# Kernel tuning notes

Measured on AMD Instinct MI355X. Metric: run time of the kernel, lower is better.

## Reference

```python
import jax, jax.numpy as jnp
import numpy as np

N_EMBED = 1024
N_HEADS = 16
HEAD_SIZE = N_EMBED // N_HEADS


def setup_inputs() -> dict:
    key = jax.random.key(0)
    ks = jax.random.split(key, 9)
    d = N_EMBED
    s = 1.0 / np.sqrt(d)
    return {
        "x": jax.random.normal(ks[0], (2, 2048, d), dtype=jnp.float32),
        "Wq": jax.random.uniform(ks[1], (d, d), jnp.float32, -s, s),
        "bq": jax.random.uniform(ks[2], (d,), jnp.float32, -s, s),
        "Wk": jax.random.uniform(ks[3], (d, d), jnp.float32, -s, s),
        "bk": jax.random.uniform(ks[4], (d,), jnp.float32, -s, s),
        "Wv": jax.random.uniform(ks[5], (d, d), jnp.float32, -s, s),
        "bv": jax.random.uniform(ks[6], (d,), jnp.float32, -s, s),
        "Wo": jax.random.uniform(ks[7], (d, d), jnp.float32, -s, s),
        "bo": jax.random.uniform(ks[8], (d,), jnp.float32, -s, s),
    }


def reference(x, Wq, bq, Wk, bk, Wv, bv, Wo, bo):
    B, T, D = x.shape
    H, Hd = N_HEADS, HEAD_SIZE
    # projections (torch Linear: x @ W^T + b; here W stored already transposed)
    q = (x @ Wq + bq).reshape(B, T, H, Hd).transpose(0, 2, 1, 3)  # [B,H,T,Hd]
    k = (x @ Wk + bk).reshape(B, T, H, Hd).transpose(0, 2, 1, 3)
    v = (x @ Wv + bv).reshape(B, T, H, Hd).transpose(0, 2, 1, 3)
    scores = jnp.einsum("bhqd,bhkd->bhqk", q, k) * (Hd ** -0.5)  # [B,H,T,T]
    causal = jnp.tril(jnp.ones((T, T), dtype=bool))
    scores = jnp.where(causal[None, None], scores, -jnp.inf)
    probs = jax.nn.softmax(scores, axis=-1)
    out = jnp.einsum("bhqk,bhkd->bhqd", probs, v)  # [B,H,T,Hd]
    out = out.transpose(0, 2, 1, 3).reshape(B, T, D)
    return out @ Wo + bo
```

## Files before the change

### kernel.cpp

```cpp
#include <hip/hip_runtime.h>
#include <cstdint>
#include <cstddef>

typedef __bf16 bf16;
typedef __bf16 bf16x4 __attribute__((ext_vector_type(4)));
typedef __bf16 bf16x8 __attribute__((ext_vector_type(8)));
typedef float  f32x4  __attribute__((ext_vector_type(4)));
typedef float  f32x16 __attribute__((ext_vector_type(16)));

#define B_  2
#define T_  2048
#define D_  1024
#define H_  16
#define HD_ 64
#define M_  (B_ * T_)
#define NQB 32

#define GLOAD_LDS(gsrc, ldst) \
    __builtin_amdgcn_global_load_lds( \
        (const __attribute__((address_space(1))) void*)(gsrc), \
        (__attribute__((address_space(3))) void*)(ldst), 16, 0, 0)

__global__ void prep_kernel(
    const float* __restrict__ x,  bf16* __restrict__ xb,
    const float* __restrict__ W0, bf16* __restrict__ T0,
    const float* __restrict__ W1, bf16* __restrict__ T1,
    const float* __restrict__ W2, bf16* __restrict__ T2,
    const float* __restrict__ W3, bf16* __restrict__ T3)
{
    if (blockIdx.z == 4) {
        const int linear = blockIdx.y * 32 + blockIdx.x;
        const int base = linear * 4096 + threadIdx.x * 4;
        #pragma unroll
        for (int u = 0; u < 4; ++u) {
            const int i = base + u * 1024;
            const float4 v = *reinterpret_cast<const float4*>(x + i);
            bf16x4 o = { (bf16)v.x, (bf16)v.y, (bf16)v.z, (bf16)v.w };
            *reinterpret_cast<bf16x4*>(xb + i) = o;
        }
        return;
    }
    __shared__ float tile[32][33];
    const float* W = blockIdx.z == 0 ? W0 : blockIdx.z == 1 ? W1 : blockIdx.z == 2 ? W2 : W3;
    bf16*       Wt = blockIdx.z == 0 ? T0 : blockIdx.z == 1 ? T1 : blockIdx.z == 2 ? T2 : T3;
    const int tx = threadIdx.x & 31, ty = threadIdx.x >> 5;
    const int bx = blockIdx.x * 32, by = blockIdx.y * 32;
    #pragma unroll
    for (int r = 0; r < 32; r += 8)
        tile[ty + r][tx] = W[(size_t)(by + ty + r) * D_ + bx + tx];
    __syncthreads();
    #pragma unroll
    for (int r = 0; r < 32; r += 8)
        Wt[(size_t)(bx + ty + r) * D_ + by + tx] = (bf16)tile[tx][ty + r];
}

__device__ __forceinline__ void gemm_128_2ph(
    const bf16* __restrict__ A, const bf16* __restrict__ Bt,
    int m0, int n0, bf16 (*As)[128][64], bf16 (*Bs)[128][64], f32x16 acc[2][2])
{
    constexpr int K = D_;
    constexpr int NK = K / 64;
    const int tid  = threadIdx.x;
    const int wave = tid >> 6, lane = tid & 63;
    const int l5 = lane & 31, hi = lane >> 5;
    const int wr = wave >> 1, wc = wave & 1;

    const int rseg = lane >> 3;
    const int srcc = (lane & 7) ^ rseg;

    auto stage = [&](int b, int k0) {
        #pragma unroll
        for (int cc = 0; cc < 4; ++cc) {
            const int c   = wave * 4 + cc;
            const int row = c * 8 + rseg;
            GLOAD_LDS(A  + (size_t)(m0 + row) * K + k0 + srcc * 8, &As[b][c * 8][0]);
            GLOAD_LDS(Bt + (size_t)(n0 + row) * K + k0 + srcc * 8, &Bs[b][c * 8][0]);
        }
    };

    stage(0, 0);
    __syncthreads();

    #pragma unroll 1
    for (int t = 0; t < NK; ++t) {
        const int cur = t & 1;
        if (t + 1 < NK) stage(cur ^ 1, (t + 1) * 64);

        bf16x8 af[2][4], bfr[2][4];
        #pragma unroll
        for (int mi = 0; mi < 2; ++mi)
            #pragma unroll
            for (int ks = 0; ks < 4; ++ks) {
                const int row = wr * 64 + mi * 32 + l5;
                af[mi][ks] = *reinterpret_cast<const bf16x8*>(
                    &As[cur][row][((ks * 2 + hi) ^ (row & 7)) * 8]);
            }
        #pragma unroll
        for (int nj = 0; nj < 2; ++nj)
            #pragma unroll
            for (int ks = 0; ks < 4; ++ks) {
                const int row = wc * 64 + nj * 32 + l5;
                bfr[nj][ks] = *reinterpret_cast<const bf16x8*>(
                    &Bs[cur][row][((ks * 2 + hi) ^ (row & 7)) * 8]);
            }
        __builtin_amdgcn_s_setprio(1);
        #pragma unroll
        for (int mi = 0; mi < 2; ++mi)
            #pragma unroll
            for (int nj = 0; nj < 2; ++nj)
                #pragma unroll
                for (int ks = 0; ks < 4; ++ks)
                    acc[mi][nj] = __builtin_amdgcn_mfma_f32_32x32x16_bf16(
                        af[mi][ks], bfr[nj][ks], acc[mi][nj], 0, 0, 0);
        __builtin_amdgcn_s_setprio(0);
        __syncthreads();
    }
}

__global__ __launch_bounds__(256, 2) void qkv128_kernel(
    const bf16* __restrict__ xb,
    const bf16* __restrict__ WqT, const float* __restrict__ bq, bf16* __restrict__ Qo,
    const bf16* __restrict__ WkT, const float* __restrict__ bk, bf16* __restrict__ Ko,
    const bf16* __restrict__ WvT, const float* __restrict__ bv, bf16* __restrict__ Vt)
{
    __shared__ bf16 As[2][128][64];
    __shared__ bf16 Bs[2][128][64];

    const int bid = blockIdx.x;
    const int swz = (bid & 7) * 96 + (bid >> 3);

    const bf16 *Aop, *Bop;
    const float *bias;
    bf16 *outp;
    float scale = 1.0f;
    int m0, n0, mode;
    if (swz < 512) {
        const int bm = swz & 31, bn = swz >> 5;
        m0 = bm * 128;
        Aop = xb;
        if (bn < 8) { Bop = WqT; n0 = bn * 128;       bias = bq; outp = Qo; scale = 0.125f; }
        else        { Bop = WkT; n0 = (bn - 8) * 128; bias = bk; outp = Ko; }
        mode = 0;
    } else {
        const int v = swz - 512, bm = v & 7, bn = v >> 3;
        m0 = bm * 128; n0 = bn * 128;
        Aop = WvT; Bop = xb; bias = bv; outp = Vt; mode = 1;
    }

    f32x16 acc[2][2] = {};
    gemm_128_2ph(Aop, Bop, m0, n0, As, Bs, acc);

    const int lane = threadIdx.x & 63, wave = threadIdx.x >> 6;
    const int l5 = lane & 31, hi = lane >> 5;
    const int wr = wave >> 1, wc = wave & 1;
    if (mode == 0) {
        #pragma unroll
        for (int mi = 0; mi < 2; ++mi)
            #pragma unroll
            for (int nj = 0; nj < 2; ++nj)
                #pragma unroll
                for (int q = 0; q < 16; ++q) {
                    const int m = m0 + wr * 64 + mi * 32 + (q & 3) + 8 * (q >> 2) + 4 * hi;
                    const int n = n0 + wc * 64 + nj * 32 + l5;
                    const float val = (acc[mi][nj][q] + bias[n]) * scale;
                    const int b = m >> 11, t = m & (T_ - 1);
                    const int h = n >> 6, hd = n & 63;
                    outp[((size_t)((b * H_ + h) * T_ + t)) * HD_ + hd] = (bf16)val;
                }
    } else {
        #pragma unroll
        for (int mi = 0; mi < 2; ++mi)
            #pragma unroll
            for (int nj = 0; nj < 2; ++nj)
                #pragma unroll
                for (int q = 0; q < 16; ++q) {
                    const int d = m0 + wr * 64 + mi * 32 + (q & 3) + 8 * (q >> 2) + 4 * hi;
                    const int n = n0 + wc * 64 + nj * 32 + l5;
                    const float val = acc[mi][nj][q] + bias[d];
                    const int b = n >> 11, t = n & (T_ - 1);
                    outp[((size_t)(b * D_ + d)) * T_ + t] = (bf16)val;
                }
    }
}

__global__ __launch_bounds__(256, 2) void gemm_out_kernel(
    const bf16* __restrict__ A, const bf16* __restrict__ WoT,
    const float* __restrict__ bo, float* __restrict__ Out)
{
    __shared__ bf16 As[2][128][64];
    __shared__ bf16 Bs[2][128][64];
    const int m0 = blockIdx.x * 128, n0 = blockIdx.y * 128;

    f32x16 acc[2][2] = {};
    gemm_128_2ph(A, WoT, m0, n0, As, Bs, acc);

    const int lane = threadIdx.x & 63, wave = threadIdx.x >> 6;
    const int l5 = lane & 31, hi = lane >> 5;
    const int wr = wave >> 1, wc = wave & 1;
    #pragma unroll
    for (int mi = 0; mi < 2; ++mi)
        #pragma unroll
        for (int nj = 0; nj < 2; ++nj)
            #pragma unroll
            for (int q = 0; q < 16; ++q) {
                const int m = m0 + wr * 64 + mi * 32 + (q & 3) + 8 * (q >> 2) + 4 * hi;
                const int n = n0 + wc * 64 + nj * 32 + l5;
                Out[(size_t)m * D_ + n] = acc[mi][nj][q] + bo[n];
            }
}

__global__ __launch_bounds__(256) void attn_kernel(
    const bf16* __restrict__ Q, const bf16* __restrict__ K,
    const bf16* __restrict__ Vt, bf16* __restrict__ Out)
{
    const int bid = blockIdx.x;
    const int xcd = bid & 7, j = bid >> 3;
    const int bh  = xcd * 4 + (j >> 4);
    const int pr  = j & 15;

    const int tid = threadIdx.x, wave = tid >> 6, lane = tid & 63;
    const int lr = lane & 15, lg = lane >> 4;
    const size_t kbase = (size_t)bh * T_ * HD_;
    const size_t vbase = (size_t)bh * HD_ * T_;

    __shared__ bf16 Ks[2][64][64];
    __shared__ bf16 Vs[2][64][64];
    __shared__ bf16 Ps[4][16][72];

    auto stage = [&](int sb, int kt) {
        const int kv0 = kt * 64;
        const int rseg = lane >> 3;
        const int srcw = (lane & 7) ^ rseg;
        #pragma unroll
        for (int cc = 0; cc < 2; ++cc) {
            const int seg = wave * 2 + cc;
            const int row = seg * 8 + rseg;
            GLOAD_LDS(K  + kbase + (size_t)(kv0 + row) * HD_ + srcw * 8, &Ks[sb][seg * 8][0]);
            GLOAD_LDS(Vt + vbase + (size_t)row * T_ + kv0 + srcw * 8,    &Vs[sb][seg * 8][0]);
        }
    };
    auto kfrag = [&](int sb, int row, int chunk) {
        return *reinterpret_cast<const bf16x8*>(&Ks[sb][row][(chunk ^ (row & 7)) * 8]);
    };
    auto vfrag = [&](int sb, int row, int chunk) {
        return *reinterpret_cast<const bf16x8*>(&Vs[sb][row][(chunk ^ (row & 7)) * 8]);
    };

    #pragma unroll 1
    for (int half = 0; half < 2; ++half) {
        const int qb = half == 0 ? pr : (NQB - 1 - pr);
        const int q0 = qb * 64;
        const int nt = qb + 1;
        const int qw = wave * 16;

        bf16x8 qf[2];
        {
            const bf16* qrow = Q + kbase + (size_t)(q0 + qw + lr) * HD_;
            qf[0] = *reinterpret_cast<const bf16x8*>(qrow + lg * 8);
            qf[1] = *reinterpret_cast<const bf16x8*>(qrow + 32 + lg * 8);
        }

        float m_s = -1e30f, l_s = 0.f;
        f32x4 o_acc[4] = {};

        stage(0, 0);
        __syncthreads();

        #pragma unroll 1
        for (int t = 0; t < nt; ++t) {
            const int cur = t & 1;
            if (t + 1 < nt) stage(cur ^ 1, t + 1);

            const int kv0 = t * 64;
            f32x4 s[4] = {};
            __builtin_amdgcn_s_setprio(1);
            #pragma unroll
            for (int n16 = 0; n16 < 4; ++n16)
                #pragma unroll
                for (int kk = 0; kk < 2; ++kk)
                    s[n16] = __builtin_amdgcn_mfma_f32_16x16x32_bf16(
                        kfrag(cur, n16 * 16 + lr, kk * 4 + lg), qf[kk], s[n16], 0, 0, 0);
            __builtin_amdgcn_s_setprio(0);
            if (t == qb) {
                #pragma unroll
                for (int n16 = 0; n16 < 4; ++n16)
                    #pragma unroll
                    for (int r = 0; r < 4; ++r)
                        if (kv0 + n16 * 16 + lg * 4 + r > q0 + qw + lr)
                            s[n16][r] = -1e30f;
            }
            float mx = s[0][0];
            #pragma unroll
            for (int n16 = 0; n16 < 4; ++n16)
                #pragma unroll
                for (int r = 0; r < 4; ++r)
                    mx = fmaxf(mx, s[n16][r]);
            mx = fmaxf(mx, __shfl_xor(mx, 16));
            mx = fmaxf(mx, __shfl_xor(mx, 32));
            if (__any(mx > m_s + 8.0f)) {
                const float mnew  = fmaxf(m_s, mx);
                const float alpha = __expf(m_s - mnew);
                #pragma unroll
                for (int r = 0; r < 4; ++r) {
                    const float a = __shfl(alpha, lg * 4 + r);
                    #pragma unroll
                    for (int nd = 0; nd < 4; ++nd) o_acc[nd][r] *= a;
                }
                l_s *= alpha;
                m_s = mnew;
            }
            float rs = 0.f;
            #pragma unroll
            for (int n16 = 0; n16 < 4; ++n16) {
                bf16x4 pw;
                #pragma unroll
                for (int r = 0; r < 4; ++r) {
                    const float p = __expf(s[n16][r] - m_s);
                    rs += p;
                    pw[r] = (bf16)p;
                }
                *reinterpret_cast<bf16x4*>(&Ps[wave][lr][n16 * 16 + lg * 4]) = pw;
            }
            rs += __shfl_xor(rs, 16);
            rs += __shfl_xor(rs, 32);
            l_s += rs;
            __builtin_amdgcn_s_setprio(1);
            #pragma unroll
            for (int ks = 0; ks < 2; ++ks) {
                const bf16x8 pa = *reinterpret_cast<const bf16x8*>(&Ps[wave][lr][ks * 32 + lg * 8]);
                #pragma unroll
                for (int nd = 0; nd < 4; ++nd)
                    o_acc[nd] = __builtin_amdgcn_mfma_f32_16x16x32_bf16(
                        pa, vfrag(cur, nd * 16 + lr, ks * 4 + lg), o_acc[nd], 0, 0, 0);
            }
            __builtin_amdgcn_s_setprio(0);
            __syncthreads();
        }

        const int b = bh >> 4, h = bh & 15;
        const float linv = 1.0f / l_s;
        #pragma unroll
        for (int r = 0; r < 4; ++r) {
            const float li = __shfl(linv, lg * 4 + r);
            const int q = q0 + qw + lg * 4 + r;
            #pragma unroll
            for (int nd = 0; nd < 4; ++nd) {
                const int d = nd * 16 + lr;
                Out[((size_t)(b * T_ + q)) * D_ + h * HD_ + d] = (bf16)(o_acc[nd][r] * li);
            }
        }
    }
}

extern "C" void kernel_launch(void* const* d_in, const int* in_sizes, int n_in,
                              void* d_out, int out_size, void* d_ws, size_t ws_size,
                              hipStream_t stream) {
    const float* x  = (const float*)d_in[0];
    const float* Wq = (const float*)d_in[1];
    const float* bq = (const float*)d_in[2];
    const float* Wk = (const float*)d_in[3];
    const float* bk = (const float*)d_in[4];
    const float* Wv = (const float*)d_in[5];
    const float* bv = (const float*)d_in[6];
    const float* Wo = (const float*)d_in[7];
    const float* bo = (const float*)d_in[8];
    float* out = (float*)d_out;

    char* ws = (char*)d_ws;
    bf16* xb   = (bf16*)(ws);
    bf16* WqT  = (bf16*)(ws + ( 8u << 20));
    bf16* WkT  = (bf16*)(ws + (10u << 20));
    bf16* WvT  = (bf16*)(ws + (12u << 20));
    bf16* WoT  = (bf16*)(ws + (14u << 20));
    bf16* Qb   = (bf16*)(ws + (16u << 20));
    bf16* Kb   = (bf16*)(ws + (24u << 20));
    bf16* Vtb  = (bf16*)(ws + (32u << 20));
    bf16* attn = (bf16*)(ws + (40u << 20));

    prep_kernel<<<dim3(32, 32, 5), 256, 0, stream>>>(
        x, xb, Wq, WqT, Wk, WkT, Wv, WvT, Wo, WoT);

    qkv128_kernel<<<768, 256, 0, stream>>>(xb, WqT, bq, Qb, WkT, bk, Kb, WvT, bv, Vtb);

    attn_kernel<<<512, 256, 0, stream>>>(Qb, Kb, Vtb, attn);

    gemm_out_kernel<<<dim3(32, 8), 256, 0, stream>>>(attn, WoT, bo, out);
}
```

Measured before the change: 126.9 us.

## Fold log2e into Q scale, split attention per q-block, retile output GEMM

The Q projection scale now includes log2(e), so the attention softmax uses exp2f directly, and the lazy-rescale threshold is scaled to match. The attention kernel drops the paired-block loop: it launches one block per (head, q-block), largest blocks first, doubling the grid to 1024 and relying on the hardware scheduler to balance the causal work. The output projection GEMM becomes a custom 64x128 tile kernel using 32x32x16 MFMA with XCD-aware swizzling and 512 blocks, aiming for better CU occupancy. More blocks add launch overhead and reload Q per block, and grid-level scheduling may balance the uneven causal work less well than the explicit pairing did.

```diff
diff --git a/kernel.cpp b/kernel.cpp
--- a/kernel.cpp
+++ b/kernel.cpp
@@ -138,7 +138,8 @@
         const int bm = swz & 31, bn = swz >> 5;
         m0 = bm * 128;
         Aop = xb;
-        if (bn < 8) { Bop = WqT; n0 = bn * 128;       bias = bq; outp = Qo; scale = 0.125f; }
+        if (bn < 8) { Bop = WqT; n0 = bn * 128;       bias = bq; outp = Qo;
+                      scale = 0.125f * 1.44269504f; }
         else        { Bop = WkT; n0 = (bn - 8) * 128; bias = bk; outp = Ko; }
         mode = 0;
     } else {
@@ -187,26 +188,78 @@
     const bf16* __restrict__ A, const bf16* __restrict__ WoT,
     const float* __restrict__ bo, float* __restrict__ Out)
 {
-    __shared__ bf16 As[2][128][64];
+    constexpr int K = D_;
+    constexpr int NK = K / 64;
+    __shared__ bf16 As[2][64][64];
     __shared__ bf16 Bs[2][128][64];
-    const int m0 = blockIdx.x * 128, n0 = blockIdx.y * 128;
-
-    f32x16 acc[2][2] = {};
-    gemm_128_2ph(A, WoT, m0, n0, As, Bs, acc);
-
-    const int lane = threadIdx.x & 63, wave = threadIdx.x >> 6;
+
+    const int bid = blockIdx.x;
+    const int swz = (bid & 7) * 64 + (bid >> 3);
+    const int m0 = (swz & 63) * 64, n0 = (swz >> 6) * 128;
+
+    const int tid = threadIdx.x, wave = tid >> 6, lane = tid & 63;
     const int l5 = lane & 31, hi = lane >> 5;
-    const int wr = wave >> 1, wc = wave & 1;
+    const int rseg = lane >> 3;
+    const int srcc = (lane & 7) ^ rseg;
+
+    auto stage = [&](int b, int k0) {
+        #pragma unroll
+        for (int cc = 0; cc < 2; ++cc) {
+            const int seg = wave * 2 + cc;
+            const int row = seg * 8 + rseg;
+            GLOAD_LDS(A + (size_t)(m0 + row) * K + k0 + srcc * 8, &As[b][seg * 8][0]);
+        }
+        #pragma unroll
+        for (int cc = 0; cc < 4; ++cc) {
+            const int seg = wave * 4 + cc;
+            const int row = seg * 8 + rseg;
+            GLOAD_LDS(WoT + (size_t)(n0 + row) * K + k0 + srcc * 8, &Bs[b][seg * 8][0]);
+        }
+    };
+
+    f32x16 acc[2] = {};
+    stage(0, 0);
+    __syncthreads();
+
+    #pragma unroll 1
+    for (int t = 0; t < NK; ++t) {
+        const int cur = t & 1;
+        if (t + 1 < NK) stage(cur ^ 1, (t + 1) * 64);
+
+        bf16x8 af[2][4], bfr[4];
+        #pragma unroll
+        for (int mi = 0; mi < 2; ++mi)
+            #pragma unroll
+            for (int ks = 0; ks < 4; ++ks) {
+                const int row = mi * 32 + l5;
+                af[mi][ks] = *reinterpret_cast<const bf16x8*>(
+                    &As[cur][row][((ks * 2 + hi) ^ (row & 7)) * 8]);
+            }
+        #pragma unroll
+        for (int ks = 0; ks < 4; ++ks) {
+            const int row = wave * 32 + l5;
+            bfr[ks] = *reinterpret_cast<const bf16x8*>(
+                &Bs[cur][row][((ks * 2 + hi) ^ (row & 7)) * 8]);
+        }
+        __builtin_amdgcn_s_setprio(1);
+        #pragma unroll
+        for (int mi = 0; mi < 2; ++mi)
+            #pragma unroll
+            for (int ks = 0; ks < 4; ++ks)
+                acc[mi] = __builtin_amdgcn_mfma_f32_32x32x16_bf16(
+                    af[mi][ks], bfr[ks], acc[mi], 0, 0, 0);
+        __builtin_amdgcn_s_setprio(0);
+        __syncthreads();
+    }
+
     #pragma unroll
     for (int mi = 0; mi < 2; ++mi)
         #pragma unroll
-        for (int nj = 0; nj < 2; ++nj)
-            #pragma unroll
-            for (int q = 0; q < 16; ++q) {
-                const int m = m0 + wr * 64 + mi * 32 + (q & 3) + 8 * (q >> 2) + 4 * hi;
-                const int n = n0 + wc * 64 + nj * 32 + l5;
-                Out[(size_t)m * D_ + n] = acc[mi][nj][q] + bo[n];
-            }
+        for (int q = 0; q < 16; ++q) {
+            const int m = m0 + mi * 32 + (q & 3) + 8 * (q >> 2) + 4 * hi;
+            const int n = n0 + wave * 32 + l5;
+            Out[(size_t)m * D_ + n] = acc[mi][q] + bo[n];
+        }
 }
 
 __global__ __launch_bounds__(256) void attn_kernel(
@@ -215,8 +268,8 @@
 {
     const int bid = blockIdx.x;
     const int xcd = bid & 7, j = bid >> 3;
-    const int bh  = xcd * 4 + (j >> 4);
-    const int pr  = j & 15;
+    const int bh  = xcd * 4 + (j >> 5);
+    const int qb  = NQB - 1 - (j & 31);
 
     const int tid = threadIdx.x, wave = tid >> 6, lane = tid & 63;
     const int lr = lane & 15, lg = lane >> 4;
@@ -246,108 +299,104 @@
         return *reinterpret_cast<const bf16x8*>(&Vs[sb][row][(chunk ^ (row & 7)) * 8]);
     };
 
+    const int q0 = qb * 64;
+    const int nt = qb + 1;
+    const int qw = wave * 16;
+
+    bf16x8 qf[2];
+    {
+        const bf16* qrow = Q + kbase + (size_t)(q0 + qw + lr) * HD_;
+        qf[0] = *reinterpret_cast<const bf16x8*>(qrow + lg * 8);
+        qf[1] = *reinterpret_cast<const bf16x8*>(qrow + 32 + lg * 8);
+    }
+
+    float m_s = -1e30f, l_s = 0.f;
+    f32x4 o_acc[4] = {};
+
+    stage(0, 0);
+    __syncthreads();
+
     #pragma unroll 1
-    for (int half = 0; half < 2; ++half) {
-        const int qb = half == 0 ? pr : (NQB - 1 - pr);
-        const int q0 = qb * 64;
-        const int nt = qb + 1;
-        const int qw = wave * 16;
-
-        bf16x8 qf[2];
-        {
-            const bf16* qrow = Q + kbase + (size_t)(q0 + qw + lr) * HD_;
-            qf[0] = *reinterpret_cast<const bf16x8*>(qrow + lg * 8);
-            qf[1] = *reinterpret_cast<const bf16x8*>(qrow + 32 + lg * 8);
-        }
-
-        float m_s = -1e30f, l_s = 0.f;
-        f32x4 o_acc[4] = {};
-
-        stage(0, 0);
-        __syncthreads();
-
-        #pragma unroll 1
-        for (int t = 0; t < nt; ++t) {
-            const int cur = t & 1;
-            if (t + 1 < nt) stage(cur ^ 1, t + 1);
-
-            const int kv0 = t * 64;
-            f32x4 s[4] = {};
-            __builtin_amdgcn_s_setprio(1);
-            #pragma unroll
-            for (int n16 = 0; n16 < 4; ++n16)
-                #pragma unroll
-                for (int kk = 0; kk < 2; ++kk)
-                    s[n16] = __builtin_amdgcn_mfma_f32_16x16x32_bf16(
-                        kfrag(cur, n16 * 16 + lr, kk * 4 + lg), qf[kk], s[n16], 0, 0, 0);
-            __builtin_amdgcn_s_setprio(0);
-            if (t == qb) {
-                #pragma unroll
-                for (int n16 = 0; n16 < 4; ++n16)
-                    #pragma unroll
-                    for (int r = 0; r < 4; ++r)
-                        if (kv0 + n16 * 16 + lg * 4 + r > q0 + qw + lr)
-                            s[n16][r] = -1e30f;
-            }
-            float mx = s[0][0];
+    for (int t = 0; t < nt; ++t) {
+        const int cur = t & 1;
+        if (t + 1 < nt) stage(cur ^ 1, t + 1);
+
+        const int kv0 = t * 64;
+        f32x4 s[4] = {};
+        __builtin_amdgcn_s_setprio(1);
+        #pragma unroll
+        for (int n16 = 0; n16 < 4; ++n16)
+            #pragma unroll
+            for (int kk = 0; kk < 2; ++kk)
+                s[n16] = __builtin_amdgcn_mfma_f32_16x16x32_bf16(
+                    kfrag(cur, n16 * 16 + lr, kk * 4 + lg), qf[kk], s[n16], 0, 0, 0);
+        __builtin_amdgcn_s_setprio(0);
+        if (t == qb) {
             #pragma unroll
             for (int n16 = 0; n16 < 4; ++n16)
                 #pragma unroll
                 for (int r = 0; r < 4; ++r)
-                    mx = fmaxf(mx, s[n16][r]);
-            mx = fmaxf(mx, __shfl_xor(mx, 16));
-            mx = fmaxf(mx, __shfl_xor(mx, 32));
-            if (__any(mx > m_s + 8.0f)) {
-                const float mnew  = fmaxf(m_s, mx);
-                const float alpha = __expf(m_s - mnew);
+                    if (kv0 + n16 * 16 + lg * 4 + r > q0 + qw + lr)
+                        s[n16][r] = -1e30f;
+        }
+        float mx = s[0][0];
+        #pragma unroll
+        for (int n16 = 0; n16 < 4; ++n16)
+            #pragma unroll
+            for (int r = 0; r < 4; ++r)
+                mx = fmaxf(mx, s[n16][r]);
+        mx = fmaxf(mx, __shfl_xor(mx, 16));
+        mx = fmaxf(mx, __shfl_xor(mx, 32));
+        if (__any(mx > m_s + 11.5416f)) {
+            const float mnew  = fmaxf(m_s, mx);
+            const float alpha = exp2f(m_s - mnew);
+            #pragma unroll
+            for (int r = 0; r < 4; ++r) {
+                const float a = __shfl(alpha, lg * 4 + r);
                 #pragma unroll
-                for (int r = 0; r < 4; ++r) {
-                    const float a = __shfl(alpha, lg * 4 + r);
-                    #pragma unroll
-                    for (int nd = 0; nd < 4; ++nd) o_acc[nd][r] *= a;
-                }
-                l_s *= alpha;
-                m_s = mnew;
+                for (int nd = 0; nd < 4; ++nd) o_acc[nd][r] *= a;
             }
-            float rs = 0.f;
-            #pragma unroll
-            for (int n16 = 0; n16 < 4; ++n16) {
-                bf16x4 pw;
-                #pragma unroll
-                for (int r = 0; r < 4; ++r) {
-                    const float p = __expf(s[n16][r] - m_s);
-                    rs += p;
-                    pw[r] = (bf16)p;
-                }
-                *reinterpret_cast<bf16x4*>(&Ps[wave][lr][n16 * 16 + lg * 4]) = pw;
+            l_s *= alpha;
+            m_s = mnew;
+        }
+        float rs = 0.f;
+        #pragma unroll
+        for (int n16 = 0; n16 < 4; ++n16) {
+            bf16x4 pw;
+            #pragma unroll
+            for (int r = 0; r < 4; ++r) {
+                const float p = exp2f(s[n16][r] - m_s);
+                rs += p;
+                pw[r] = (bf16)p;
             }
-            rs += __shfl_xor(rs, 16);
-            rs += __shfl_xor(rs, 32);
-            l_s += rs;
-            __builtin_amdgcn_s_setprio(1);
-            #pragma unroll
-            for (int ks = 0; ks < 2; ++ks) {
-                const bf16x8 pa = *reinterpret_cast<const bf16x8*>(&Ps[wave][lr][ks * 32 + lg * 8]);
-                #pragma unroll
-                for (int nd = 0; nd < 4; ++nd)
-                    o_acc[nd] = __builtin_amdgcn_mfma_f32_16x16x32_bf16(
-                        pa, vfrag(cur, nd * 16 + lr, ks * 4 + lg), o_acc[nd], 0, 0, 0);
-            }
-            __builtin_amdgcn_s_setprio(0);
-            __syncthreads();
-        }
-
-        const int b = bh >> 4, h = bh & 15;
-        const float linv = 1.0f / l_s;
-        #pragma unroll
-        for (int r = 0; r < 4; ++r) {
-            const float li = __shfl(linv, lg * 4 + r);
-            const int q = q0 + qw + lg * 4 + r;
-            #pragma unroll
-            for (int nd = 0; nd < 4; ++nd) {
-                const int d = nd * 16 + lr;
-                Out[((size_t)(b * T_ + q)) * D_ + h * HD_ + d] = (bf16)(o_acc[nd][r] * li);
-            }
+            *reinterpret_cast<bf16x4*>(&Ps[wave][lr][n16 * 16 + lg * 4]) = pw;
+        }
+        rs += __shfl_xor(rs, 16);
+        rs += __shfl_xor(rs, 32);
+        l_s += rs;
+        __builtin_amdgcn_s_setprio(1);
+        #pragma unroll
+        for (int ks = 0; ks < 2; ++ks) {
+            const bf16x8 pa = *reinterpret_cast<const bf16x8*>(&Ps[wave][lr][ks * 32 + lg * 8]);
+            #pragma unroll
+            for (int nd = 0; nd < 4; ++nd)
+                o_acc[nd] = __builtin_amdgcn_mfma_f32_16x16x32_bf16(
+                    pa, vfrag(cur, nd * 16 + lr, ks * 4 + lg), o_acc[nd], 0, 0, 0);
+        }
+        __builtin_amdgcn_s_setprio(0);
+        __syncthreads();
+    }
+
+    const int b = bh >> 4, h = bh & 15;
+    const float linv = 1.0f / l_s;
+    #pragma unroll
+    for (int r = 0; r < 4; ++r) {
+        const float li = __shfl(linv, lg * 4 + r);
+        const int q = q0 + qw + lg * 4 + r;
+        #pragma unroll
+        for (int nd = 0; nd < 4; ++nd) {
+            const int d = nd * 16 + lr;
+            Out[((size_t)(b * T_ + q)) * D_ + h * HD_ + d] = (bf16)(o_acc[nd][r] * li);
         }
     }
 }
@@ -382,7 +431,7 @@
 
     qkv128_kernel<<<768, 256, 0, stream>>>(xb, WqT, bq, Qb, WkT, bk, Kb, WvT, bv, Vtb);
 
-    attn_kernel<<<512, 256, 0, stream>>>(Qb, Kb, Vtb, attn);
-
-    gemm_out_kernel<<<dim3(32, 8), 256, 0, stream>>>(attn, WoT, bo, out);
-}
+    attn_kernel<<<1024, 256, 0, stream>>>(Qb, Kb, Vtb, attn);
+
+    gemm_out_kernel<<<512, 256, 0, stream>>>(attn, WoT, bo, out);
+}
```

Result: slower. 139.8 us (+10.2%).
